# Optimization experiments

Hardware: AMD Instinct MI355X
Metric: run time of the kernel (lower is better)

The kernel has to match this reference:

```python
import jax, jax.numpy as jnp
import numpy as np

D_MODEL = 1024
NUM_HEADS = 16
HEAD_DIM = D_MODEL // NUM_HEADS
WINDOW = 64
BATCH = 2
SEQ = 2048


def setup_inputs() -> dict:
    key = jax.random.key(0)
    ks = jax.random.split(key, 5)
    s = 1.0 / np.sqrt(D_MODEL)  # torch Linear-ish init scale
    x = jax.random.normal(ks[0], (BATCH, SEQ, D_MODEL), dtype=jnp.float32)
    Wq = jax.random.normal(ks[1], (D_MODEL, D_MODEL), dtype=jnp.float32) * s
    Wk = jax.random.normal(ks[2], (D_MODEL, D_MODEL), dtype=jnp.float32) * s
    Wv = jax.random.normal(ks[3], (D_MODEL, D_MODEL), dtype=jnp.float32) * s
    Wo = jax.random.normal(ks[4], (D_MODEL, D_MODEL), dtype=jnp.float32) * s
    z = jnp.zeros((D_MODEL,), dtype=jnp.float32)
    return {"x": x, "Wq": Wq, "bq": z, "Wk": Wk, "bk": z, "Wv": Wv, "bv": z,
            "Wo": Wo, "bo": z}


def reference(x, Wq, bq, Wk, bk, Wv, bv, Wo, bo):
    B, S, D = x.shape
    H, Hd = NUM_HEADS, HEAD_DIM
    # QKV projections; weights stored as [in, out] so y = x @ W + b
    q = (x @ Wq + bq).reshape(B, S, H, Hd).transpose(0, 2, 1, 3)  # bhsd
    k = (x @ Wk + bk).reshape(B, S, H, Hd).transpose(0, 2, 1, 3)
    v = (x @ Wv + bv).reshape(B, S, H, Hd).transpose(0, 2, 1, 3)
    scores = jnp.einsum('bhqd,bhkd->bhqk', q, k) / jnp.sqrt(jnp.float32(Hd))
    # static local-window band mask: attend only where |i - j| <= window_size
    idx = jnp.arange(S)
    dist = jnp.abs(idx[None, :] - idx[:, None])  # [S, S]
    scores = jnp.where(dist[None, None] > WINDOW, -jnp.inf, scores)
    attn = jax.nn.softmax(scores, axis=-1)
    out = jnp.einsum('bhqk,bhkd->bhqd', attn, v)
    out = out.transpose(0, 2, 1, 3).reshape(B, S, D)
    return out @ Wo + bo
```

## Files before the change

kernel.cpp:

```cpp
#include <hip/hip_runtime.h>
#include <cstdint>
#include <cstddef>

typedef __bf16 bf16x8 __attribute__((ext_vector_type(8)));
typedef float  f32x4  __attribute__((ext_vector_type(4)));

__device__ __forceinline__ unsigned short f2bf(float f) {
    union { __bf16 b; unsigned short u; } cv; cv.b = (__bf16)f; return cv.u;
}
__device__ __forceinline__ int iclamp(int v, int lo, int hi) {
    return v < lo ? lo : (v > hi ? hi : v);
}

__device__ __forceinline__ void gload16(const void* gsrc, void* ldsdst) {
    __builtin_amdgcn_global_load_lds(
        (const __attribute__((address_space(1))) unsigned int*)(uintptr_t)gsrc,
        (__attribute__((address_space(3))) unsigned int*)(uintptr_t)ldsdst,
        16, 0, 0);
}

#define MFMA16(a, b, c) __builtin_amdgcn_mfma_f32_16x16x32_bf16((a), (b), (c), 0, 0, 0)

__global__ __launch_bounds__(256) void prep_k(const float* __restrict__ x,
                                              const float* __restrict__ Wq,
                                              const float* __restrict__ Wk,
                                              const float* __restrict__ Wv,
                                              const float* __restrict__ Wo,
                                              const float* __restrict__ bq,
                                              const float* __restrict__ bk,
                                              const float* __restrict__ bv,
                                              unsigned short* __restrict__ xb,
                                              unsigned short* __restrict__ Wt,
                                              float* __restrict__ bc) {
    __shared__ float tile[64][65];
    const int bx = blockIdx.x, tid = threadIdx.x;
    if (bx < 1024) {
        const int z = bx >> 8, t = bx & 255;
        const float* W = (z == 0) ? Wq : (z == 1) ? Wk : (z == 2) ? Wv : Wo;
        const int n0 = (t & 15) * 64, k0 = (t >> 4) * 64;
        const int tr = tid >> 4, tc = (tid & 15) * 4;
#pragma unroll
        for (int i = 0; i < 4; ++i) {
            int r = tr + i * 16;
            float4 v = *(const float4*)(W + (size_t)(k0 + r) * 1024 + n0 + tc);
            tile[r][tc + 0] = v.x; tile[r][tc + 1] = v.y;
            tile[r][tc + 2] = v.z; tile[r][tc + 3] = v.w;
        }
        __syncthreads();
        const int n = tid & 63, kc = (tid >> 6) * 16;
        union { unsigned short u[16]; uint4 q[2]; } pk;
#pragma unroll
        for (int c = 0; c < 16; ++c) pk.u[c] = f2bf(tile[kc + c][n]);
        uint4* dst = (uint4*)(Wt + (size_t)z * 1048576 + (size_t)(n0 + n) * 1024 + k0 + kc);
        dst[0] = pk.q[0]; dst[1] = pk.q[1];
    } else if (bx < 3072) {
        size_t i = ((size_t)(bx - 1024) * 256 + tid) * 8;
        float4 a = *(const float4*)(x + i);
        float4 b = *(const float4*)(x + i + 4);
        union { unsigned short u[8]; uint4 q; } pk;
        pk.u[0] = f2bf(a.x); pk.u[1] = f2bf(a.y); pk.u[2] = f2bf(a.z); pk.u[3] = f2bf(a.w);
        pk.u[4] = f2bf(b.x); pk.u[5] = f2bf(b.y); pk.u[6] = f2bf(b.z); pk.u[7] = f2bf(b.w);
        *(uint4*)(xb + i) = pk.q;
    } else {
        int i = (bx - 3072) * 256 + tid;
        bc[i] = (i < 1024) ? bq[i] : (i < 2048) ? bk[i - 1024] : bv[i - 2048];
    }
}


#define QKV_BAR   __builtin_amdgcn_s_barrier()
#define QKV_SB0   __builtin_amdgcn_sched_barrier(0)
#define QKV_LGKM0 asm volatile("s_waitcnt lgkmcnt(0)" ::: "memory")
#define QKV_VM7   asm volatile("s_waitcnt vmcnt(7)" ::: "memory")
#define QKV_VM0   asm volatile("s_waitcnt vmcnt(0)" ::: "memory")
#define QKV_PRIO1 __builtin_amdgcn_s_setprio(1)
#define QKV_PRIO0 __builtin_amdgcn_s_setprio(0)

#define PHASE_READS(AB, I0)                                                    \
    af00 = *(const bf16x8*)((AB) + aRow + (I0) * 1024 + sw0);                  \
    af01 = *(const bf16x8*)((AB) + aRow + (I0) * 1024 + sw1);                  \
    af10 = *(const bf16x8*)((AB) + aRow + (I0) * 1024 + 1024 + sw0);           \
    af11 = *(const bf16x8*)((AB) + aRow + (I0) * 1024 + 1024 + sw1);

#define PHASE_MFMA(I0)                                                         \
    acc[(I0)][0]     = MFMA16(af00, b00, acc[(I0)][0]);                        \
    acc[(I0)][0]     = MFMA16(af01, b10, acc[(I0)][0]);                        \
    acc[(I0)][1]     = MFMA16(af00, b01, acc[(I0)][1]);                        \
    acc[(I0)][1]     = MFMA16(af01, b11, acc[(I0)][1]);                        \
    acc[(I0)][2]     = MFMA16(af00, b02, acc[(I0)][2]);                        \
    acc[(I0)][2]     = MFMA16(af01, b12, acc[(I0)][2]);                        \
    acc[(I0) + 1][0] = MFMA16(af10, b00, acc[(I0) + 1][0]);                    \
    acc[(I0) + 1][0] = MFMA16(af11, b10, acc[(I0) + 1][0]);                    \
    acc[(I0) + 1][1] = MFMA16(af10, b01, acc[(I0) + 1][1]);                    \
    acc[(I0) + 1][1] = MFMA16(af11, b11, acc[(I0) + 1][1]);                    \
    acc[(I0) + 1][2] = MFMA16(af10, b02, acc[(I0) + 1][2]);                    \
    acc[(I0) + 1][2] = MFMA16(af11, b12, acc[(I0) + 1][2]);

#define STAGE_T(BOA, BOB, KT) do {                                             \
    gload16(gA0 + (KT), lA0 + (BOA)); gload16(gA1 + (KT), lA1 + (BOA));        \
    gload16(gA2 + (KT), lA2 + (BOA)); gload16(gA3 + (KT), lA3 + (BOA));        \
    gload16(gB0 + (KT), lB0 + (BOB)); gload16(gB1 + (KT), lB1 + (BOB));        \
    gload16(gB2 + (KT), lB2 + (BOB)); } while (0)

#define KTILE(AB, BB, BOA, BOB, T) do {                                        \
    bf16x8 af00, af01, af10, af11;                                             \
    bf16x8 b00, b10, b01, b11, b02, b12;                                       \
    b00 = *(const bf16x8*)((BB) + bRow + sw0);                                 \
    b10 = *(const bf16x8*)((BB) + bRow + sw1);                                 \
    b01 = *(const bf16x8*)((BB) + bRow + 1024 + sw0);                          \
    b11 = *(const bf16x8*)((BB) + bRow + 1024 + sw1);                          \
    b02 = *(const bf16x8*)((BB) + bRow + 2048 + sw0);                          \
    b12 = *(const bf16x8*)((BB) + bRow + 2048 + sw1);                          \
    PHASE_READS(AB, 0);                                                        \
    QKV_BAR; QKV_LGKM0; QKV_SB0;                                               \
    QKV_PRIO1; PHASE_MFMA(0); QKV_PRIO0; QKV_BAR;                              \
    PHASE_READS(AB, 2);                                                        \
    QKV_BAR; QKV_LGKM0; QKV_SB0;                                               \
    QKV_PRIO1; PHASE_MFMA(2); QKV_PRIO0; QKV_BAR;                              \
    PHASE_READS(AB, 4);                                                        \
    QKV_BAR; QKV_LGKM0; QKV_SB0;                                               \
    QKV_PRIO1; PHASE_MFMA(4); QKV_PRIO0; QKV_BAR;                              \
    PHASE_READS(AB, 6);                                                        \
    QKV_LGKM0; QKV_SB0; QKV_BAR;                                               \
    if ((T) < 14) STAGE_T((BOA), (BOB), (T) * 64 + 128);                       \
    QKV_PRIO1; PHASE_MFMA(6); QKV_PRIO0;                                       \
    if ((T) < 14)      { QKV_VM7; QKV_SB0; QKV_BAR; }                          \
    else if ((T) < 15) { QKV_VM0; QKV_SB0; QKV_BAR; }                          \
} while (0)

__global__ __launch_bounds__(512, 2) void gemm_qkv(const unsigned short* __restrict__ xb,
                                                   const unsigned short* __restrict__ Wt,
                                                   const float* __restrict__ bcat,
                                                   unsigned short* __restrict__ Qb,
                                                   unsigned short* __restrict__ Kb,
                                                   unsigned short* __restrict__ Vt) {
    __shared__ __align__(16) unsigned short Asm[2 * 256 * 64];
    __shared__ __align__(16) unsigned short Bsm[2 * 192 * 64];
    const int tid = threadIdx.x, wave = tid >> 6, lane = tid & 63;
    const int lq = lane & 15, quad = lane >> 4;
    const int wr = wave >> 2, wc = wave & 3;
    const int m0 = blockIdx.x * 256, n0 = blockIdx.y * 192;

    f32x4 acc[8][3];
#pragma unroll
    for (int i = 0; i < 8; ++i)
#pragma unroll
        for (int j = 0; j < 3; ++j) acc[i][j] = f32x4{0.f, 0.f, 0.f, 0.f};

    float bi[3];
#pragma unroll
    for (int j = 0; j < 3; ++j) bi[j] = bcat[n0 + wc * 48 + j * 16 + lq];

    const int r8 = lane >> 3, cs = lane & 7;
    const int gch = (cs ^ r8) * 8;
    const unsigned short* gA0 = xb + (size_t)(m0 +   0 + wave * 8 + r8) * 1024 + gch;
    const unsigned short* gA1 = xb + (size_t)(m0 +  64 + wave * 8 + r8) * 1024 + gch;
    const unsigned short* gA2 = xb + (size_t)(m0 + 128 + wave * 8 + r8) * 1024 + gch;
    const unsigned short* gA3 = xb + (size_t)(m0 + 192 + wave * 8 + r8) * 1024 + gch;
    const unsigned short* gB0 = Wt + (size_t)(n0 +   0 + wave * 8 + r8) * 1024 + gch;
    const unsigned short* gB1 = Wt + (size_t)(n0 +  64 + wave * 8 + r8) * 1024 + gch;
    const unsigned short* gB2 = Wt + (size_t)(n0 + 128 + wave * 8 + r8) * 1024 + gch;
    unsigned short* lA0 = Asm + (  0 + wave * 8) * 64;
    unsigned short* lA1 = Asm + ( 64 + wave * 8) * 64;
    unsigned short* lA2 = Asm + (128 + wave * 8) * 64;
    unsigned short* lA3 = Asm + (192 + wave * 8) * 64;
    unsigned short* lB0 = Bsm + (  0 + wave * 8) * 64;
    unsigned short* lB1 = Bsm + ( 64 + wave * 8) * 64;
    unsigned short* lB2 = Bsm + (128 + wave * 8) * 64;

    const int sw0 = ((quad)     ^ (lq & 7)) * 8;
    const int sw1 = ((4 + quad) ^ (lq & 7)) * 8;
    const int aRow = (wr * 128 + lq) * 64;
    const int bRow = (wc * 48  + lq) * 64;

    STAGE_T(0, 0, 0);
    STAGE_T(16384, 12288, 64);
    QKV_VM7; QKV_SB0; QKV_BAR;

    for (int u = 0; u < 8; ++u) {
        const int t0 = u * 2;
        KTILE(Asm,          Bsm,          0,     0,     t0);
        KTILE(Asm + 16384,  Bsm + 12288,  16384, 12288, t0 + 1);
    }

    const int b = m0 >> 11;
    const int mb = (m0 & 2047) + wr * 128;
    unsigned short* sw = Asm + wave * 1024;
    const int row32 = lane >> 1, half = lane & 1;
#pragma unroll
    for (int i = 0; i < 8; ++i) {
#pragma unroll
        for (int j = 0; j < 3; ++j)
#pragma unroll
            for (int r = 0; r < 4; ++r)
                sw[(quad * 4 + r) * 56 + j * 16 + lq] = f2bf(acc[i][j][r] + bi[j]);
        const int sb = mb + i * 16;
#pragma unroll
        for (int j = 0; j < 3; ++j) {
            const int c0 = n0 + wc * 48 + j * 16;
            const int p = c0 >> 10, ch = c0 & 1023;
            const int h = ch >> 6, d0 = ch & 63;
            if (p < 2) {
                unsigned short* base = (p == 0) ? Qb : Kb;
                if (lane < 32) {
                    uint4 v = *(const uint4*)(sw + row32 * 56 + j * 16 + half * 8);
                    *(uint4*)(base + ((size_t)((b * 16 + h) * 2048 + sb + row32)) * 64
                              + d0 + half * 8) = v;
                }
            } else {
                if (lane < 32) {
                    union { unsigned short u[8]; uint4 q; } pk;
#pragma unroll
                    for (int q2 = 0; q2 < 8; ++q2)
                        pk.u[q2] = sw[(half * 8 + q2) * 56 + j * 16 + row32];
                    *(uint4*)(Vt + ((size_t)((b * 16 + h) * 64 + d0 + row32)) * 2048
                              + sb + half * 8) = pk.q;
                }
            }
        }
    }
}

__global__ __launch_bounds__(256, 4) void attn_k(const unsigned short* __restrict__ Qb,
                                                 const unsigned short* __restrict__ Kb,
                                                 const unsigned short* __restrict__ Vt,
                                                 unsigned short* __restrict__ AO) {
    __shared__ __align__(16) unsigned short P[4][16 * 168];
    const int tid = threadIdx.x, wave = tid >> 6, lane = tid & 63;
    const int lq = lane & 15, quad = lane >> 4;
    const int b = blockIdx.z, h = blockIdx.y;
    const int q0 = blockIdx.x * 64 + wave * 16;
    const bool edge = (blockIdx.x == 0) || (blockIdx.x == 31);
    const unsigned short* Qh = Qb + (size_t)((b * 16 + h) * 2048) * 64;
    const unsigned short* Kh = Kb + (size_t)((b * 16 + h) * 2048) * 64;
    const unsigned short* Vh = Vt + (size_t)((b * 16 + h) * 64) * 2048;
    unsigned short* pw = P[wave];

    {
        unsigned int* zp = (unsigned int*)(pw + (lane >> 2) * 168 + 144 + (lane & 3) * 4);
        zp[0] = 0u; zp[1] = 0u;
    }

    const bf16x8 qa0 = *(const bf16x8*)(Qh + (size_t)(q0 + lq) * 64 + quad * 8);
    const bf16x8 qa1 = *(const bf16x8*)(Qh + (size_t)(q0 + lq) * 64 + 32 + quad * 8);

    float pr[9][4];
    float ls[4] = {0.f, 0.f, 0.f, 0.f};
#pragma unroll
    for (int t = 0; t < 9; ++t) {
        const int krow = q0 - 64 + t * 16 + lq;
        const bool need_mask = (t == 0) || (t == 8) || edge;
        const int krc = need_mask ? iclamp(krow, 0, 2047) : krow;
        const unsigned short* kp = Kh + (size_t)krc * 64 + quad * 8;
        const bf16x8 kf0 = *(const bf16x8*)kp;
        const bf16x8 kf1 = *(const bf16x8*)(kp + 32);
        f32x4 cacc = f32x4{0.f, 0.f, 0.f, 0.f};
        cacc = MFMA16(qa0, kf0, cacc);
        cacc = MFMA16(qa1, kf1, cacc);
        if (need_mask) {
#pragma unroll
            for (int r = 0; r < 4; ++r) {
                const int q = q0 + quad * 4 + r;
                const int dj = q - krow;
                const bool ok = (krow >= 0) && (krow < 2048) && (dj <= 64) && (dj >= -64);
                const float pv = ok ? __expf(cacc[r] * 0.125f) : 0.f;
                pr[t][r] = pv;
                ls[r] += pv;
            }
        } else {
#pragma unroll
            for (int r = 0; r < 4; ++r) {
                const float pv = __expf(cacc[r] * 0.125f);
                pr[t][r] = pv;
                ls[r] += pv;
            }
        }
    }
#pragma unroll
    for (int r = 0; r < 4; ++r) {
#pragma unroll
        for (int off = 1; off < 16; off <<= 1)
            ls[r] += __shfl_xor(ls[r], off);
    }
    float rinv[4];
#pragma unroll
    for (int r = 0; r < 4; ++r) rinv[r] = 1.f / ls[r];

#pragma unroll
    for (int t = 0; t < 9; ++t)
#pragma unroll
        for (int r = 0; r < 4; ++r)
            pw[(quad * 4 + r) * 168 + t * 16 + lq] = f2bf(pr[t][r]);

    f32x4 oa[4];
#pragma unroll
    for (int dt = 0; dt < 4; ++dt) oa[dt] = f32x4{0.f, 0.f, 0.f, 0.f};
#pragma unroll
    for (int ks = 0; ks < 5; ++ks) {
        const bf16x8 pf = *(const bf16x8*)(pw + lq * 168 + ks * 32 + quad * 8);
        int s0 = q0 - 64 + ks * 32 + quad * 8;
        s0 = iclamp(s0, 0, 2040);
#pragma unroll
        for (int dt = 0; dt < 4; ++dt) {
            const bf16x8 vf = *(const bf16x8*)(Vh + (size_t)(dt * 16 + lq) * 2048 + s0);
            oa[dt] = MFMA16(pf, vf, oa[dt]);
        }
    }

#pragma unroll
    for (int dt = 0; dt < 4; ++dt)
#pragma unroll
        for (int r = 0; r < 4; ++r)
            pw[(quad * 4 + r) * 72 + dt * 16 + lq] = f2bf(oa[dt][r] * rinv[r]);
    {
        const int row = lane >> 2, c0 = (lane & 3) * 16;
        uint4 v0 = *(const uint4*)(pw + row * 72 + c0);
        uint4 v1 = *(const uint4*)(pw + row * 72 + c0 + 8);
        unsigned short* dp = AO + (size_t)(b * 2048 + q0 + row) * 1024 + h * 64 + c0;
        *(uint4*)(dp) = v0;
        *(uint4*)(dp + 8) = v1;
    }
}

__global__ __launch_bounds__(256, 2) void gemm_out(const unsigned short* __restrict__ AO,
                                                   const unsigned short* __restrict__ Wot,
                                                   const float* __restrict__ bo,
                                                   float* __restrict__ out) {
    __shared__ __align__(16) unsigned short Asm[128 * 64];
    __shared__ __align__(16) unsigned short Bsm[64 * 64];
    const int tid = threadIdx.x, wave = tid >> 6, lane = tid & 63;
    const int lq = lane & 15, quad = lane >> 4;
    const int m0 = blockIdx.y * 128, n0 = blockIdx.x * 64;

    f32x4 acc[4][2];
#pragma unroll
    for (int i = 0; i < 4; ++i)
#pragma unroll
        for (int j = 0; j < 2; ++j) acc[i][j] = f32x4{0.f, 0.f, 0.f, 0.f};

    float bi[2];
#pragma unroll
    for (int j = 0; j < 2; ++j) bi[j] = bo[n0 + (wave & 1) * 32 + j * 16 + lq];

    const int r8 = lane >> 3, cs = lane & 7;
    const int gch = (cs ^ r8) * 8;
    const unsigned short* gA[4];
    unsigned short* lA[4];
#pragma unroll
    for (int s = 0; s < 4; ++s) {
        const int r = wave * 32 + s * 8 + r8;
        gA[s] = AO + (size_t)(m0 + r) * 1024 + gch;
        lA[s] = Asm + (wave * 32 + s * 8) * 64;
    }
    const unsigned short* gB[2];
    unsigned short* lB[2];
#pragma unroll
    for (int s = 0; s < 2; ++s) {
        const int r = wave * 16 + s * 8 + r8;
        gB[s] = Wot + (size_t)(n0 + r) * 1024 + gch;
        lB[s] = Bsm + (wave * 16 + s * 8) * 64;
    }

    int offA[4][2], offB[2][2];
#pragma unroll
    for (int kk = 0; kk < 2; ++kk) {
#pragma unroll
        for (int i = 0; i < 4; ++i) {
            const int rA = (wave >> 1) * 64 + i * 16 + lq;
            offA[i][kk] = rA * 64 + (((kk * 4 + quad) ^ (lq & 7)) * 8);
        }
#pragma unroll
        for (int j = 0; j < 2; ++j) {
            const int rB = (wave & 1) * 32 + j * 16 + lq;
            offB[j][kk] = rB * 64 + (((kk * 4 + quad) ^ (lq & 7)) * 8);
        }
    }

    for (int kt = 0; kt < 1024; kt += 64) {
#pragma unroll
        for (int s = 0; s < 4; ++s) gload16(gA[s] + kt, lA[s]);
#pragma unroll
        for (int s = 0; s < 2; ++s) gload16(gB[s] + kt, lB[s]);
        __syncthreads();
#pragma unroll
        for (int kk = 0; kk < 2; ++kk) {
            bf16x8 af[4], bfr[2];
#pragma unroll
            for (int i = 0; i < 4; ++i) af[i] = *(const bf16x8*)(Asm + offA[i][kk]);
#pragma unroll
            for (int j = 0; j < 2; ++j) bfr[j] = *(const bf16x8*)(Bsm + offB[j][kk]);
#pragma unroll
            for (int i = 0; i < 4; ++i)
#pragma unroll
                for (int j = 0; j < 2; ++j)
                    acc[i][j] = MFMA16(af[i], bfr[j], acc[i][j]);
        }
        __syncthreads();
    }

    float* swf = (float*)Asm + wave * 528;
    const int row = lane >> 2, c0 = (lane & 3) * 8;
    const size_t obase = (size_t)(m0 + (wave >> 1) * 64) * 1024 + n0 + (wave & 1) * 32;
#pragma unroll
    for (int i = 0; i < 4; ++i) {
#pragma unroll
        for (int j = 0; j < 2; ++j)
#pragma unroll
            for (int r = 0; r < 4; ++r)
                swf[(quad * 4 + r) * 33 + j * 16 + lq] = acc[i][j][r] + bi[j];
        float4 v0, v1;
        v0.x = swf[row * 33 + c0 + 0]; v0.y = swf[row * 33 + c0 + 1];
        v0.z = swf[row * 33 + c0 + 2]; v0.w = swf[row * 33 + c0 + 3];
        v1.x = swf[row * 33 + c0 + 4]; v1.y = swf[row * 33 + c0 + 5];
        v1.z = swf[row * 33 + c0 + 6]; v1.w = swf[row * 33 + c0 + 7];
        float* op = out + obase + (size_t)(i * 16 + row) * 1024 + c0;
        *(float4*)(op) = v0;
        *(float4*)(op + 4) = v1;
    }
}

extern "C" void kernel_launch(void* const* d_in, const int* in_sizes, int n_in,
                              void* d_out, int out_size, void* d_ws, size_t ws_size,
                              hipStream_t stream) {
    const float* x  = (const float*)d_in[0];
    const float* Wq = (const float*)d_in[1];
    const float* bq = (const float*)d_in[2];
    const float* Wk = (const float*)d_in[3];
    const float* bk = (const float*)d_in[4];
    const float* Wv = (const float*)d_in[5];
    const float* bv = (const float*)d_in[6];
    const float* Wo = (const float*)d_in[7];
    const float* bo = (const float*)d_in[8];
    float* out = (float*)d_out;

    unsigned short* us = (unsigned short*)d_ws;
    const size_t MEG = 1048576;
    unsigned short* xb = us;
    unsigned short* Wt = us + 4 * MEG;
    unsigned short* Qb = us + 8 * MEG;
    unsigned short* Kb = us + 12 * MEG;
    unsigned short* Vt = us + 16 * MEG;
    unsigned short* AO = us + 20 * MEG;
    float* bcat = (float*)(us + 24 * MEG);

    prep_k<<<3084, 256, 0, stream>>>(x, Wq, Wk, Wv, Wo, bq, bk, bv, xb, Wt, bcat);
    gemm_qkv<<<dim3(16, 16), 512, 0, stream>>>(xb, Wt, bcat, Qb, Kb, Vt);
    attn_k<<<dim3(32, 16, 2), 256, 0, stream>>>(Qb, Kb, Vt, AO);
    gemm_out<<<dim3(16, 32), 256, 0, stream>>>(AO, Wt + 3 * MEG, bo, out);
}
```

Baseline: 161.2 us.

## Fuse all four stages into one persistent cooperative kernel with grid syncs

Replaces the four separate launches (conversion, QKV GEMM, windowed attention, output GEMM) with one cooperative kernel of 256 blocks of 512 threads. The stages are separated by grid-wide syncs and share one LDS buffer. Each stage remaps its work onto the fixed grid: the attention stage gives each wave one 16-query task, and the output GEMM gives each 256-thread half-block one tile. This removes inter-kernel launch gaps. The cost is grid-sync overhead, fixed occupancy per stage, and a different work split that may reduce per-stage efficiency. The old multi-kernel path is kept as a fallback if the cooperative launch fails.

```diff
diff --git a/kernel.cpp b/kernel.cpp
--- a/kernel.cpp
+++ b/kernel.cpp
@@ -1,6 +1,9 @@
 #include <hip/hip_runtime.h>
+#include <hip/hip_cooperative_groups.h>
 #include <cstdint>
 #include <cstddef>
+
+namespace cg = cooperative_groups;
 
 typedef __bf16 bf16x8 __attribute__((ext_vector_type(8)));
 typedef float  f32x4  __attribute__((ext_vector_type(4)));
@@ -20,53 +23,6 @@
 }
 
 #define MFMA16(a, b, c) __builtin_amdgcn_mfma_f32_16x16x32_bf16((a), (b), (c), 0, 0, 0)
-
-__global__ __launch_bounds__(256) void prep_k(const float* __restrict__ x,
-                                              const float* __restrict__ Wq,
-                                              const float* __restrict__ Wk,
-                                              const float* __restrict__ Wv,
-                                              const float* __restrict__ Wo,
-                                              const float* __restrict__ bq,
-                                              const float* __restrict__ bk,
-                                              const float* __restrict__ bv,
-                                              unsigned short* __restrict__ xb,
-                                              unsigned short* __restrict__ Wt,
-                                              float* __restrict__ bc) {
-    __shared__ float tile[64][65];
-    const int bx = blockIdx.x, tid = threadIdx.x;
-    if (bx < 1024) {
-        const int z = bx >> 8, t = bx & 255;
-        const float* W = (z == 0) ? Wq : (z == 1) ? Wk : (z == 2) ? Wv : Wo;
-        const int n0 = (t & 15) * 64, k0 = (t >> 4) * 64;
-        const int tr = tid >> 4, tc = (tid & 15) * 4;
-#pragma unroll
-        for (int i = 0; i < 4; ++i) {
-            int r = tr + i * 16;
-            float4 v = *(const float4*)(W + (size_t)(k0 + r) * 1024 + n0 + tc);
-            tile[r][tc + 0] = v.x; tile[r][tc + 1] = v.y;
-            tile[r][tc + 2] = v.z; tile[r][tc + 3] = v.w;
-        }
-        __syncthreads();
-        const int n = tid & 63, kc = (tid >> 6) * 16;
-        union { unsigned short u[16]; uint4 q[2]; } pk;
-#pragma unroll
-        for (int c = 0; c < 16; ++c) pk.u[c] = f2bf(tile[kc + c][n]);
-        uint4* dst = (uint4*)(Wt + (size_t)z * 1048576 + (size_t)(n0 + n) * 1024 + k0 + kc);
-        dst[0] = pk.q[0]; dst[1] = pk.q[1];
-    } else if (bx < 3072) {
-        size_t i = ((size_t)(bx - 1024) * 256 + tid) * 8;
-        float4 a = *(const float4*)(x + i);
-        float4 b = *(const float4*)(x + i + 4);
-        union { unsigned short u[8]; uint4 q; } pk;
-        pk.u[0] = f2bf(a.x); pk.u[1] = f2bf(a.y); pk.u[2] = f2bf(a.z); pk.u[3] = f2bf(a.w);
-        pk.u[4] = f2bf(b.x); pk.u[5] = f2bf(b.y); pk.u[6] = f2bf(b.z); pk.u[7] = f2bf(b.w);
-        *(uint4*)(xb + i) = pk.q;
-    } else {
-        int i = (bx - 3072) * 256 + tid;
-        bc[i] = (i < 1024) ? bq[i] : (i < 2048) ? bk[i - 1024] : bv[i - 2048];
-    }
-}
-
 
 #define QKV_BAR   __builtin_amdgcn_s_barrier()
 #define QKV_SB0   __builtin_amdgcn_sched_barrier(0)
@@ -128,6 +84,404 @@
     else if ((T) < 15) { QKV_VM0; QKV_SB0; QKV_BAR; }                          \
 } while (0)
 
+__global__ __launch_bounds__(512, 2) void fused_all(
+        const float* __restrict__ x,  const float* __restrict__ Wq,
+        const float* __restrict__ Wk, const float* __restrict__ Wv,
+        const float* __restrict__ Wo, const float* __restrict__ bq,
+        const float* __restrict__ bk, const float* __restrict__ bv,
+        const float* __restrict__ bo, float* __restrict__ out,
+        unsigned short* __restrict__ us) {
+    __shared__ __align__(16) char LDSU[114688];
+    const int bx = blockIdx.x, tid = threadIdx.x;
+    const int wave = tid >> 6, lane = tid & 63;
+    const int lq = lane & 15, quad = lane >> 4;
+    const int grp = tid >> 8, ltid = tid & 255;
+
+    const size_t MEG = 1048576;
+    unsigned short* xb = us;
+    unsigned short* Wt = us + 4 * MEG;
+    unsigned short* Qb = us + 8 * MEG;
+    unsigned short* Kb = us + 12 * MEG;
+    unsigned short* Vt = us + 16 * MEG;
+    unsigned short* AO = us + 20 * MEG;
+    float* bcat = (float*)(us + 24 * MEG);
+
+    {
+        float (*tile)[65] = (float(*)[65])(LDSU + grp * 16640);
+        for (int it = 0; it < 7; ++it) {
+            const int vb = bx * 2 + grp + it * 512;
+            int z = 0, t = 0, n0 = 0, k0 = 0;
+            bool isW = false;
+            if (vb < 1024) {
+                isW = true;
+                z = vb >> 8; t = vb & 255;
+                n0 = (t & 15) * 64; k0 = (t >> 4) * 64;
+                const float* W = (z == 0) ? Wq : (z == 1) ? Wk : (z == 2) ? Wv : Wo;
+                const int tr = ltid >> 4, tc = (ltid & 15) * 4;
+#pragma unroll
+                for (int i = 0; i < 4; ++i) {
+                    int r = tr + i * 16;
+                    float4 v = *(const float4*)(W + (size_t)(k0 + r) * 1024 + n0 + tc);
+                    tile[r][tc + 0] = v.x; tile[r][tc + 1] = v.y;
+                    tile[r][tc + 2] = v.z; tile[r][tc + 3] = v.w;
+                }
+            } else if (vb < 3072) {
+                size_t i = ((size_t)(vb - 1024) * 256 + ltid) * 8;
+                float4 a = *(const float4*)(x + i);
+                float4 b2 = *(const float4*)(x + i + 4);
+                union { unsigned short u[8]; uint4 q; } pk;
+                pk.u[0] = f2bf(a.x);  pk.u[1] = f2bf(a.y);
+                pk.u[2] = f2bf(a.z);  pk.u[3] = f2bf(a.w);
+                pk.u[4] = f2bf(b2.x); pk.u[5] = f2bf(b2.y);
+                pk.u[6] = f2bf(b2.z); pk.u[7] = f2bf(b2.w);
+                *(uint4*)(xb + i) = pk.q;
+            } else if (vb < 3084) {
+                int i = (vb - 3072) * 256 + ltid;
+                bcat[i] = (i < 1024) ? bq[i] : (i < 2048) ? bk[i - 1024] : bv[i - 2048];
+            }
+            __syncthreads();
+            if (isW) {
+                const int n = ltid & 63, kc = (ltid >> 6) * 16;
+                union { unsigned short u[16]; uint4 q[2]; } pk;
+#pragma unroll
+                for (int c = 0; c < 16; ++c) pk.u[c] = f2bf(tile[kc + c][n]);
+                uint4* dst = (uint4*)(Wt + (size_t)z * 1048576 + (size_t)(n0 + n) * 1024 + k0 + kc);
+                dst[0] = pk.q[0]; dst[1] = pk.q[1];
+            }
+            __syncthreads();
+        }
+    }
+    cg::this_grid().sync();
+
+    {
+        unsigned short* Asm = (unsigned short*)LDSU;
+        unsigned short* Bsm = (unsigned short*)(LDSU + 65536);
+        const int wr = wave >> 2, wc = wave & 3;
+        const int m0 = (bx >> 4) * 256;
+        const int n0 = ((bx & 7) * 2 + ((bx >> 3) & 1)) * 192;
+
+        f32x4 acc[8][3];
+#pragma unroll
+        for (int i = 0; i < 8; ++i)
+#pragma unroll
+            for (int j = 0; j < 3; ++j) acc[i][j] = f32x4{0.f, 0.f, 0.f, 0.f};
+
+        float bi[3];
+#pragma unroll
+        for (int j = 0; j < 3; ++j) bi[j] = bcat[n0 + wc * 48 + j * 16 + lq];
+
+        const int r8 = lane >> 3, cs = lane & 7;
+        const int gch = (cs ^ r8) * 8;
+        const unsigned short* gA0 = xb + (size_t)(m0 +   0 + wave * 8 + r8) * 1024 + gch;
+        const unsigned short* gA1 = xb + (size_t)(m0 +  64 + wave * 8 + r8) * 1024 + gch;
+        const unsigned short* gA2 = xb + (size_t)(m0 + 128 + wave * 8 + r8) * 1024 + gch;
+        const unsigned short* gA3 = xb + (size_t)(m0 + 192 + wave * 8 + r8) * 1024 + gch;
+        const unsigned short* gB0 = Wt + (size_t)(n0 +   0 + wave * 8 + r8) * 1024 + gch;
+        const unsigned short* gB1 = Wt + (size_t)(n0 +  64 + wave * 8 + r8) * 1024 + gch;
+        const unsigned short* gB2 = Wt + (size_t)(n0 + 128 + wave * 8 + r8) * 1024 + gch;
+        unsigned short* lA0 = Asm + (  0 + wave * 8) * 64;
+        unsigned short* lA1 = Asm + ( 64 + wave * 8) * 64;
+        unsigned short* lA2 = Asm + (128 + wave * 8) * 64;
+        unsigned short* lA3 = Asm + (192 + wave * 8) * 64;
+        unsigned short* lB0 = Bsm + (  0 + wave * 8) * 64;
+        unsigned short* lB1 = Bsm + ( 64 + wave * 8) * 64;
+        unsigned short* lB2 = Bsm + (128 + wave * 8) * 64;
+
+        const int sw0 = ((quad)     ^ (lq & 7)) * 8;
+        const int sw1 = ((4 + quad) ^ (lq & 7)) * 8;
+        const int aRow = (wr * 128 + lq) * 64;
+        const int bRow = (wc * 48  + lq) * 64;
+
+        STAGE_T(0, 0, 0);
+        STAGE_T(16384, 12288, 64);
+        QKV_VM7; QKV_SB0; QKV_BAR;
+
+        for (int u = 0; u < 8; ++u) {
+            const int t0 = u * 2;
+            KTILE(Asm,         Bsm,         0,     0,     t0);
+            KTILE(Asm + 16384, Bsm + 12288, 16384, 12288, t0 + 1);
+        }
+
+        const int b = m0 >> 11;
+        const int mb = (m0 & 2047) + wr * 128;
+        unsigned short* sw = Asm + wave * 1024;
+        const int row32 = lane >> 1, half = lane & 1;
+#pragma unroll
+        for (int i = 0; i < 8; ++i) {
+#pragma unroll
+            for (int j = 0; j < 3; ++j)
+#pragma unroll
+                for (int r = 0; r < 4; ++r)
+                    sw[(quad * 4 + r) * 56 + j * 16 + lq] = f2bf(acc[i][j][r] + bi[j]);
+            const int sb = mb + i * 16;
+#pragma unroll
+            for (int j = 0; j < 3; ++j) {
+                const int c0 = n0 + wc * 48 + j * 16;
+                const int p = c0 >> 10, ch = c0 & 1023;
+                const int h = ch >> 6, d0 = ch & 63;
+                if (p < 2) {
+                    unsigned short* base = (p == 0) ? Qb : Kb;
+                    if (lane < 32) {
+                        uint4 v = *(const uint4*)(sw + row32 * 56 + j * 16 + half * 8);
+                        *(uint4*)(base + ((size_t)((b * 16 + h) * 2048 + sb + row32)) * 64
+                                  + d0 + half * 8) = v;
+                    }
+                } else {
+                    if (lane < 32) {
+                        union { unsigned short u[8]; uint4 q; } pk;
+#pragma unroll
+                        for (int q2 = 0; q2 < 8; ++q2)
+                            pk.u[q2] = sw[(half * 8 + q2) * 56 + j * 16 + row32];
+                        *(uint4*)(Vt + ((size_t)((b * 16 + h) * 64 + d0 + row32)) * 2048
+                                  + sb + half * 8) = pk.q;
+                    }
+                }
+            }
+        }
+    }
+    cg::this_grid().sync();
+
+    {
+        unsigned short* pw = ((unsigned short*)LDSU) + wave * (16 * 168);
+        for (int rep = 0; rep < 2; ++rep) {
+            const int task = bx * 8 + wave + rep * 2048;
+            const int b = task >> 11, h = (task >> 7) & 15, qt = task & 127;
+            const int q0 = qt * 16;
+            const bool edge = (qt < 4) || (qt >= 124);
+            const unsigned short* Qh = Qb + (size_t)((b * 16 + h) * 2048) * 64;
+            const unsigned short* Kh = Kb + (size_t)((b * 16 + h) * 2048) * 64;
+            const unsigned short* Vh = Vt + (size_t)((b * 16 + h) * 64) * 2048;
+
+            {
+                unsigned int* zp = (unsigned int*)(pw + (lane >> 2) * 168 + 144 + (lane & 3) * 4);
+                zp[0] = 0u; zp[1] = 0u;
+            }
+
+            const bf16x8 qa0 = *(const bf16x8*)(Qh + (size_t)(q0 + lq) * 64 + quad * 8);
+            const bf16x8 qa1 = *(const bf16x8*)(Qh + (size_t)(q0 + lq) * 64 + 32 + quad * 8);
+
+            float pr[9][4];
+            float ls[4] = {0.f, 0.f, 0.f, 0.f};
+#pragma unroll
+            for (int t = 0; t < 9; ++t) {
+                const int krow = q0 - 64 + t * 16 + lq;
+                const bool need_mask = (t == 0) || (t == 8) || edge;
+                const int krc = need_mask ? iclamp(krow, 0, 2047) : krow;
+                const unsigned short* kp = Kh + (size_t)krc * 64 + quad * 8;
+                const bf16x8 kf0 = *(const bf16x8*)kp;
+                const bf16x8 kf1 = *(const bf16x8*)(kp + 32);
+                f32x4 cacc = f32x4{0.f, 0.f, 0.f, 0.f};
+                cacc = MFMA16(qa0, kf0, cacc);
+                cacc = MFMA16(qa1, kf1, cacc);
+                if (need_mask) {
+#pragma unroll
+                    for (int r = 0; r < 4; ++r) {
+                        const int q = q0 + quad * 4 + r;
+                        const int dj = q - krow;
+                        const bool ok = (krow >= 0) && (krow < 2048) && (dj <= 64) && (dj >= -64);
+                        const float pv = ok ? __expf(cacc[r] * 0.125f) : 0.f;
+                        pr[t][r] = pv;
+                        ls[r] += pv;
+                    }
+                } else {
+#pragma unroll
+                    for (int r = 0; r < 4; ++r) {
+                        const float pv = __expf(cacc[r] * 0.125f);
+                        pr[t][r] = pv;
+                        ls[r] += pv;
+                    }
+                }
+            }
+#pragma unroll
+            for (int r = 0; r < 4; ++r) {
+#pragma unroll
+                for (int off = 1; off < 16; off <<= 1)
+                    ls[r] += __shfl_xor(ls[r], off);
+            }
+            float rinv[4];
+#pragma unroll
+            for (int r = 0; r < 4; ++r) rinv[r] = 1.f / ls[r];
+
+#pragma unroll
+            for (int t = 0; t < 9; ++t)
+#pragma unroll
+                for (int r = 0; r < 4; ++r)
+                    pw[(quad * 4 + r) * 168 + t * 16 + lq] = f2bf(pr[t][r]);
+
+            f32x4 oa[4];
+#pragma unroll
+            for (int dt = 0; dt < 4; ++dt) oa[dt] = f32x4{0.f, 0.f, 0.f, 0.f};
+#pragma unroll
+            for (int ks = 0; ks < 5; ++ks) {
+                const bf16x8 pf = *(const bf16x8*)(pw + lq * 168 + ks * 32 + quad * 8);
+                int s0 = q0 - 64 + ks * 32 + quad * 8;
+                s0 = iclamp(s0, 0, 2040);
+#pragma unroll
+                for (int dt = 0; dt < 4; ++dt) {
+                    const bf16x8 vf = *(const bf16x8*)(Vh + (size_t)(dt * 16 + lq) * 2048 + s0);
+                    oa[dt] = MFMA16(pf, vf, oa[dt]);
+                }
+            }
+
+#pragma unroll
+            for (int dt = 0; dt < 4; ++dt)
+#pragma unroll
+                for (int r = 0; r < 4; ++r)
+                    pw[(quad * 4 + r) * 72 + dt * 16 + lq] = f2bf(oa[dt][r] * rinv[r]);
+            {
+                const int row = lane >> 2, c0 = (lane & 3) * 16;
+                uint4 v0 = *(const uint4*)(pw + row * 72 + c0);
+                uint4 v1 = *(const uint4*)(pw + row * 72 + c0 + 8);
+                unsigned short* dp = AO + (size_t)(b * 2048 + q0 + row) * 1024 + h * 64 + c0;
+                *(uint4*)(dp) = v0;
+                *(uint4*)(dp + 8) = v1;
+            }
+        }
+    }
+    cg::this_grid().sync();
+
+    {
+        unsigned short* AsmO = (unsigned short*)(LDSU + grp * 24576);
+        unsigned short* BsmO = AsmO + 128 * 64;
+        const unsigned short* Wot = Wt + 3 * MEG;
+        const int wv = wave & 3;
+        const int vb = bx * 2 + grp;
+        const int m0 = (vb >> 4) * 128, n0 = (vb & 15) * 64;
+
+        f32x4 acc[4][2];
+#pragma unroll
+        for (int i = 0; i < 4; ++i)
+#pragma unroll
+            for (int j = 0; j < 2; ++j) acc[i][j] = f32x4{0.f, 0.f, 0.f, 0.f};
+
+        float bi[2];
+#pragma unroll
+        for (int j = 0; j < 2; ++j) bi[j] = bo[n0 + (wv & 1) * 32 + j * 16 + lq];
+
+        const int r8 = lane >> 3, cs = lane & 7;
+        const int gch = (cs ^ r8) * 8;
+        const unsigned short* gA[4];
+        unsigned short* lA[4];
+#pragma unroll
+        for (int s = 0; s < 4; ++s) {
+            const int r = wv * 32 + s * 8 + r8;
+            gA[s] = AO + (size_t)(m0 + r) * 1024 + gch;
+            lA[s] = AsmO + (wv * 32 + s * 8) * 64;
+        }
+        const unsigned short* gB[2];
+        unsigned short* lB[2];
+#pragma unroll
+        for (int s = 0; s < 2; ++s) {
+            const int r = wv * 16 + s * 8 + r8;
+            gB[s] = Wot + (size_t)(n0 + r) * 1024 + gch;
+            lB[s] = BsmO + (wv * 16 + s * 8) * 64;
+        }
+
+        int offA[4][2], offB[2][2];
+#pragma unroll
+        for (int kk = 0; kk < 2; ++kk) {
+#pragma unroll
+            for (int i = 0; i < 4; ++i) {
+                const int rA = (wv >> 1) * 64 + i * 16 + lq;
+                offA[i][kk] = rA * 64 + (((kk * 4 + quad) ^ (lq & 7)) * 8);
+            }
+#pragma unroll
+            for (int j = 0; j < 2; ++j) {
+                const int rB = (wv & 1) * 32 + j * 16 + lq;
+                offB[j][kk] = rB * 64 + (((kk * 4 + quad) ^ (lq & 7)) * 8);
+            }
+        }
+
+        for (int kt = 0; kt < 1024; kt += 64) {
+#pragma unroll
+            for (int s = 0; s < 4; ++s) gload16(gA[s] + kt, lA[s]);
+#pragma unroll
+            for (int s = 0; s < 2; ++s) gload16(gB[s] + kt, lB[s]);
+            __syncthreads();
+#pragma unroll
+            for (int kk = 0; kk < 2; ++kk) {
+                bf16x8 af[4], bfr[2];
+#pragma unroll
+                for (int i = 0; i < 4; ++i) af[i] = *(const bf16x8*)(AsmO + offA[i][kk]);
+#pragma unroll
+                for (int j = 0; j < 2; ++j) bfr[j] = *(const bf16x8*)(BsmO + offB[j][kk]);
+#pragma unroll
+                for (int i = 0; i < 4; ++i)
+#pragma unroll
+                    for (int j = 0; j < 2; ++j)
+                        acc[i][j] = MFMA16(af[i], bfr[j], acc[i][j]);
+            }
+            __syncthreads();
+        }
+
+        float* swf = (float*)AsmO + wv * 528;
+        const int row = lane >> 2, c0 = (lane & 3) * 8;
+        const size_t obase = (size_t)(m0 + (wv >> 1) * 64) * 1024 + n0 + (wv & 1) * 32;
+#pragma unroll
+        for (int i = 0; i < 4; ++i) {
+#pragma unroll
+            for (int j = 0; j < 2; ++j)
+#pragma unroll
+                for (int r = 0; r < 4; ++r)
+                    swf[(quad * 4 + r) * 33 + j * 16 + lq] = acc[i][j][r] + bi[j];
+            float4 v0, v1;
+            v0.x = swf[row * 33 + c0 + 0]; v0.y = swf[row * 33 + c0 + 1];
+            v0.z = swf[row * 33 + c0 + 2]; v0.w = swf[row * 33 + c0 + 3];
+            v1.x = swf[row * 33 + c0 + 4]; v1.y = swf[row * 33 + c0 + 5];
+            v1.z = swf[row * 33 + c0 + 6]; v1.w = swf[row * 33 + c0 + 7];
+            float* op = out + obase + (size_t)(i * 16 + row) * 1024 + c0;
+            *(float4*)(op) = v0;
+            *(float4*)(op + 4) = v1;
+        }
+    }
+}
+
+__global__ __launch_bounds__(256) void prep_k(const float* __restrict__ x,
+                                              const float* __restrict__ Wq,
+                                              const float* __restrict__ Wk,
+                                              const float* __restrict__ Wv,
+                                              const float* __restrict__ Wo,
+                                              const float* __restrict__ bq,
+                                              const float* __restrict__ bk,
+                                              const float* __restrict__ bv,
+                                              unsigned short* __restrict__ xb,
+                                              unsigned short* __restrict__ Wt,
+                                              float* __restrict__ bc) {
+    __shared__ float tile[64][65];
+    const int bx = blockIdx.x, tid = threadIdx.x;
+    if (bx < 1024) {
+        const int z = bx >> 8, t = bx & 255;
+        const float* W = (z == 0) ? Wq : (z == 1) ? Wk : (z == 2) ? Wv : Wo;
+        const int n0 = (t & 15) * 64, k0 = (t >> 4) * 64;
+        const int tr = tid >> 4, tc = (tid & 15) * 4;
+#pragma unroll
+        for (int i = 0; i < 4; ++i) {
+            int r = tr + i * 16;
+            float4 v = *(const float4*)(W + (size_t)(k0 + r) * 1024 + n0 + tc);
+            tile[r][tc + 0] = v.x; tile[r][tc + 1] = v.y;
+            tile[r][tc + 2] = v.z; tile[r][tc + 3] = v.w;
+        }
+        __syncthreads();
+        const int n = tid & 63, kc = (tid >> 6) * 16;
+        union { unsigned short u[16]; uint4 q[2]; } pk;
+#pragma unroll
+        for (int c = 0; c < 16; ++c) pk.u[c] = f2bf(tile[kc + c][n]);
+        uint4* dst = (uint4*)(Wt + (size_t)z * 1048576 + (size_t)(n0 + n) * 1024 + k0 + kc);
+        dst[0] = pk.q[0]; dst[1] = pk.q[1];
+    } else if (bx < 3072) {
+        size_t i = ((size_t)(bx - 1024) * 256 + tid) * 8;
+        float4 a = *(const float4*)(x + i);
+        float4 b = *(const float4*)(x + i + 4);
+        union { unsigned short u[8]; uint4 q; } pk;
+        pk.u[0] = f2bf(a.x); pk.u[1] = f2bf(a.y); pk.u[2] = f2bf(a.z); pk.u[3] = f2bf(a.w);
+        pk.u[4] = f2bf(b.x); pk.u[5] = f2bf(b.y); pk.u[6] = f2bf(b.z); pk.u[7] = f2bf(b.w);
+        *(uint4*)(xb + i) = pk.q;
+    } else {
+        int i = (bx - 3072) * 256 + tid;
+        bc[i] = (i < 1024) ? bq[i] : (i < 2048) ? bk[i - 1024] : bv[i - 2048];
+    }
+}
+
 __global__ __launch_bounds__(512, 2) void gemm_qkv(const unsigned short* __restrict__ xb,
                                                    const unsigned short* __restrict__ Wt,
                                                    const float* __restrict__ bcat,
@@ -432,19 +786,28 @@
     const float* Wo = (const float*)d_in[7];
     const float* bo = (const float*)d_in[8];
     float* out = (float*)d_out;
-
     unsigned short* us = (unsigned short*)d_ws;
-    const size_t MEG = 1048576;
-    unsigned short* xb = us;
-    unsigned short* Wt = us + 4 * MEG;
-    unsigned short* Qb = us + 8 * MEG;
-    unsigned short* Kb = us + 12 * MEG;
-    unsigned short* Vt = us + 16 * MEG;
-    unsigned short* AO = us + 20 * MEG;
-    float* bcat = (float*)(us + 24 * MEG);
-
-    prep_k<<<3084, 256, 0, stream>>>(x, Wq, Wk, Wv, Wo, bq, bk, bv, xb, Wt, bcat);
-    gemm_qkv<<<dim3(16, 16), 512, 0, stream>>>(xb, Wt, bcat, Qb, Kb, Vt);
-    attn_k<<<dim3(32, 16, 2), 256, 0, stream>>>(Qb, Kb, Vt, AO);
-    gemm_out<<<dim3(16, 32), 256, 0, stream>>>(AO, Wt + 3 * MEG, bo, out);
+
+    void* args[11];
+    args[0] = (void*)&x;  args[1] = (void*)&Wq; args[2] = (void*)&Wk;
+    args[3] = (void*)&Wv; args[4] = (void*)&Wo; args[5] = (void*)&bq;
+    args[6] = (void*)&bk; args[7] = (void*)&bv; args[8] = (void*)&bo;
+    args[9] = (void*)&out; args[10] = (void*)&us;
+
+    hipError_t e = hipLaunchCooperativeKernel((const void*)fused_all, dim3(256), dim3(512),
+                                              args, 0, stream);
+    if (e != hipSuccess) {
+        const size_t MEG = 1048576;
+        unsigned short* xb = us;
+        unsigned short* Wt = us + 4 * MEG;
+        unsigned short* Qb = us + 8 * MEG;
+        unsigned short* Kb = us + 12 * MEG;
+        unsigned short* Vt = us + 16 * MEG;
+        unsigned short* AO = us + 20 * MEG;
+        float* bcat = (float*)(us + 24 * MEG);
+        prep_k<<<3084, 256, 0, stream>>>(x, Wq, Wk, Wv, Wo, bq, bk, bv, xb, Wt, bcat);
+        gemm_qkv<<<dim3(16, 16), 512, 0, stream>>>(xb, Wt, bcat, Qb, Kb, Vt);
+        attn_k<<<dim3(32, 16, 2), 256, 0, stream>>>(Qb, Kb, Vt, AO);
+        gemm_out<<<dim3(16, 32), 256, 0, stream>>>(AO, Wt + 3 * MEG, bo, out);
+    }
 }
```

After: 283.6 us. +75.9%, slower.

## Double-buffer output GEMM with 128x128 tiles and interleaved prefetch schedule

Applied to the files above, without the earlier changes.

Rewrites the output projection GEMM to use 512-thread blocks computing 128x128 tiles instead of 256-thread 128x64 tiles, which halves the grid and doubles B-tile reuse. The main loop now keeps a two-stage LDS ring: the next-but-one k-tile is prefetched with direct global-to-LDS loads while MFMAs run on the current buffer. It uses explicit waitcnt, barriers and setprio, following the QKV GEMM's schedule. The cost is more LDS per block and fewer blocks (256) across the CUs.

```diff
diff --git a/kernel.cpp b/kernel.cpp
--- a/kernel.cpp
+++ b/kernel.cpp
@@ -67,11 +67,11 @@
     }
 }
 
-
 #define QKV_BAR   __builtin_amdgcn_s_barrier()
 #define QKV_SB0   __builtin_amdgcn_sched_barrier(0)
 #define QKV_LGKM0 asm volatile("s_waitcnt lgkmcnt(0)" ::: "memory")
 #define QKV_VM7   asm volatile("s_waitcnt vmcnt(7)" ::: "memory")
+#define QKV_VM4   asm volatile("s_waitcnt vmcnt(4)" ::: "memory")
 #define QKV_VM0   asm volatile("s_waitcnt vmcnt(0)" ::: "memory")
 #define QKV_PRIO1 __builtin_amdgcn_s_setprio(1)
 #define QKV_PRIO0 __builtin_amdgcn_s_setprio(0)
@@ -322,15 +322,54 @@
     }
 }
 
-__global__ __launch_bounds__(256, 2) void gemm_out(const unsigned short* __restrict__ AO,
+
+#define STAGE_O(BO, KT) do {                                                   \
+    gload16(gAo0 + (KT), lAo0 + (BO)); gload16(gAo1 + (KT), lAo1 + (BO));      \
+    gload16(gBo0 + (KT), lBo0 + (BO)); gload16(gBo1 + (KT), lBo1 + (BO)); } while (0)
+
+#define KTILE_O(AB, BB, BO, T) do {                                            \
+    bf16x8 a00, a01, a10, a11, b00, b10, b01, b11;                             \
+    b00 = *(const bf16x8*)((BB) + bRow + sw0);                                 \
+    b10 = *(const bf16x8*)((BB) + bRow + sw1);                                 \
+    b01 = *(const bf16x8*)((BB) + bRow + 1024 + sw0);                          \
+    b11 = *(const bf16x8*)((BB) + bRow + 1024 + sw1);                          \
+    a00 = *(const bf16x8*)((AB) + aRow + sw0);                                 \
+    a01 = *(const bf16x8*)((AB) + aRow + sw1);                                 \
+    a10 = *(const bf16x8*)((AB) + aRow + 1024 + sw0);                          \
+    a11 = *(const bf16x8*)((AB) + aRow + 1024 + sw1);                          \
+    QKV_BAR; QKV_LGKM0; QKV_SB0;                                               \
+    QKV_PRIO1;                                                                 \
+    acc[0][0]=MFMA16(a00,b00,acc[0][0]); acc[0][0]=MFMA16(a01,b10,acc[0][0]);  \
+    acc[0][1]=MFMA16(a00,b01,acc[0][1]); acc[0][1]=MFMA16(a01,b11,acc[0][1]);  \
+    acc[1][0]=MFMA16(a10,b00,acc[1][0]); acc[1][0]=MFMA16(a11,b10,acc[1][0]);  \
+    acc[1][1]=MFMA16(a10,b01,acc[1][1]); acc[1][1]=MFMA16(a11,b11,acc[1][1]);  \
+    QKV_PRIO0; QKV_BAR;                                                        \
+    a00 = *(const bf16x8*)((AB) + aRow + 2048 + sw0);                          \
+    a01 = *(const bf16x8*)((AB) + aRow + 2048 + sw1);                          \
+    a10 = *(const bf16x8*)((AB) + aRow + 3072 + sw0);                          \
+    a11 = *(const bf16x8*)((AB) + aRow + 3072 + sw1);                          \
+    QKV_LGKM0; QKV_SB0; QKV_BAR;                                               \
+    if ((T) < 14) STAGE_O((BO), (T) * 64 + 128);                               \
+    QKV_PRIO1;                                                                 \
+    acc[2][0]=MFMA16(a00,b00,acc[2][0]); acc[2][0]=MFMA16(a01,b10,acc[2][0]);  \
+    acc[2][1]=MFMA16(a00,b01,acc[2][1]); acc[2][1]=MFMA16(a01,b11,acc[2][1]);  \
+    acc[3][0]=MFMA16(a10,b00,acc[3][0]); acc[3][0]=MFMA16(a11,b10,acc[3][0]);  \
+    acc[3][1]=MFMA16(a10,b01,acc[3][1]); acc[3][1]=MFMA16(a11,b11,acc[3][1]);  \
+    QKV_PRIO0;                                                                 \
+    if ((T) < 14)      { QKV_VM4; QKV_SB0; QKV_BAR; }                          \
+    else if ((T) < 15) { QKV_VM0; QKV_SB0; QKV_BAR; }                          \
+} while (0)
+
+__global__ __launch_bounds__(512, 2) void gemm_out(const unsigned short* __restrict__ AO,
                                                    const unsigned short* __restrict__ Wot,
                                                    const float* __restrict__ bo,
                                                    float* __restrict__ out) {
-    __shared__ __align__(16) unsigned short Asm[128 * 64];
-    __shared__ __align__(16) unsigned short Bsm[64 * 64];
+    __shared__ __align__(16) unsigned short Asm[2 * 128 * 64];
+    __shared__ __align__(16) unsigned short Bsm[2 * 128 * 64];
     const int tid = threadIdx.x, wave = tid >> 6, lane = tid & 63;
     const int lq = lane & 15, quad = lane >> 4;
-    const int m0 = blockIdx.y * 128, n0 = blockIdx.x * 64;
+    const int wr = wave >> 2, wc = wave & 3;
+    const int m0 = blockIdx.y * 128, n0 = blockIdx.x * 128;
 
     f32x4 acc[4][2];
 #pragma unroll
@@ -340,67 +379,38 @@
 
     float bi[2];
 #pragma unroll
-    for (int j = 0; j < 2; ++j) bi[j] = bo[n0 + (wave & 1) * 32 + j * 16 + lq];
+    for (int j = 0; j < 2; ++j) bi[j] = bo[n0 + wc * 32 + j * 16 + lq];
 
     const int r8 = lane >> 3, cs = lane & 7;
     const int gch = (cs ^ r8) * 8;
-    const unsigned short* gA[4];
-    unsigned short* lA[4];
-#pragma unroll
-    for (int s = 0; s < 4; ++s) {
-        const int r = wave * 32 + s * 8 + r8;
-        gA[s] = AO + (size_t)(m0 + r) * 1024 + gch;
-        lA[s] = Asm + (wave * 32 + s * 8) * 64;
-    }
-    const unsigned short* gB[2];
-    unsigned short* lB[2];
-#pragma unroll
-    for (int s = 0; s < 2; ++s) {
-        const int r = wave * 16 + s * 8 + r8;
-        gB[s] = Wot + (size_t)(n0 + r) * 1024 + gch;
-        lB[s] = Bsm + (wave * 16 + s * 8) * 64;
-    }
-
-    int offA[4][2], offB[2][2];
-#pragma unroll
-    for (int kk = 0; kk < 2; ++kk) {
-#pragma unroll
-        for (int i = 0; i < 4; ++i) {
-            const int rA = (wave >> 1) * 64 + i * 16 + lq;
-            offA[i][kk] = rA * 64 + (((kk * 4 + quad) ^ (lq & 7)) * 8);
-        }
-#pragma unroll
-        for (int j = 0; j < 2; ++j) {
-            const int rB = (wave & 1) * 32 + j * 16 + lq;
-            offB[j][kk] = rB * 64 + (((kk * 4 + quad) ^ (lq & 7)) * 8);
-        }
-    }
-
-    for (int kt = 0; kt < 1024; kt += 64) {
-#pragma unroll
-        for (int s = 0; s < 4; ++s) gload16(gA[s] + kt, lA[s]);
-#pragma unroll
-        for (int s = 0; s < 2; ++s) gload16(gB[s] + kt, lB[s]);
-        __syncthreads();
-#pragma unroll
-        for (int kk = 0; kk < 2; ++kk) {
-            bf16x8 af[4], bfr[2];
-#pragma unroll
-            for (int i = 0; i < 4; ++i) af[i] = *(const bf16x8*)(Asm + offA[i][kk]);
-#pragma unroll
-            for (int j = 0; j < 2; ++j) bfr[j] = *(const bf16x8*)(Bsm + offB[j][kk]);
-#pragma unroll
-            for (int i = 0; i < 4; ++i)
-#pragma unroll
-                for (int j = 0; j < 2; ++j)
-                    acc[i][j] = MFMA16(af[i], bfr[j], acc[i][j]);
-        }
-        __syncthreads();
-    }
-
+    const unsigned short* gAo0 = AO  + (size_t)(m0 +  0 + wave * 8 + r8) * 1024 + gch;
+    const unsigned short* gAo1 = AO  + (size_t)(m0 + 64 + wave * 8 + r8) * 1024 + gch;
+    const unsigned short* gBo0 = Wot + (size_t)(n0 +  0 + wave * 8 + r8) * 1024 + gch;
+    const unsigned short* gBo1 = Wot + (size_t)(n0 + 64 + wave * 8 + r8) * 1024 + gch;
+    unsigned short* lAo0 = Asm + ( 0 + wave * 8) * 64;
+    unsigned short* lAo1 = Asm + (64 + wave * 8) * 64;
+    unsigned short* lBo0 = Bsm + ( 0 + wave * 8) * 64;
+    unsigned short* lBo1 = Bsm + (64 + wave * 8) * 64;
+
+    const int sw0 = ((quad)     ^ (lq & 7)) * 8;
+    const int sw1 = ((4 + quad) ^ (lq & 7)) * 8;
+    const int aRow = (wr * 64 + lq) * 64;
+    const int bRow = (wc * 32 + lq) * 64;
+
+    STAGE_O(0, 0);
+    STAGE_O(8192, 64);
+    QKV_VM4; QKV_SB0; QKV_BAR;
+
+    for (int u = 0; u < 8; ++u) {
+        const int t0 = u * 2;
+        KTILE_O(Asm,        Bsm,        0,    t0);
+        KTILE_O(Asm + 8192, Bsm + 8192, 8192, t0 + 1);
+    }
+
+    __syncthreads();
     float* swf = (float*)Asm + wave * 528;
     const int row = lane >> 2, c0 = (lane & 3) * 8;
-    const size_t obase = (size_t)(m0 + (wave >> 1) * 64) * 1024 + n0 + (wave & 1) * 32;
+    const size_t obase = (size_t)(m0 + wr * 64) * 1024 + n0 + wc * 32;
 #pragma unroll
     for (int i = 0; i < 4; ++i) {
 #pragma unroll
@@ -446,5 +456,5 @@
     prep_k<<<3084, 256, 0, stream>>>(x, Wq, Wk, Wv, Wo, bq, bk, bv, xb, Wt, bcat);
     gemm_qkv<<<dim3(16, 16), 512, 0, stream>>>(xb, Wt, bcat, Qb, Kb, Vt);
     attn_k<<<dim3(32, 16, 2), 256, 0, stream>>>(Qb, Kb, Vt, AO);
-    gemm_out<<<dim3(16, 32), 256, 0, stream>>>(AO, Wt + 3 * MEG, bo, out);
-}
+    gemm_out<<<dim3(8, 32), 512, 0, stream>>>(AO, Wt + 3 * MEG, bo, out);
+}
```

Measured after the change: 160.2 us. No clear change (-0.6%).
